# Kernel optimization log

Measured on AMD Instinct MI355X. Metric: run time of the kernel, lower is better.

Reference implementation:

```python
import jax, jax.numpy as jnp
import numpy as np

H = 64        # num_attention_heads
HK = 8        # num_key_value_heads
HD = 64       # head_dim
DM = 1024     # hidden_size
WINDOW = 128  # sliding_window


def setup_inputs() -> dict:
    key = jax.random.key(0)
    ks = jax.random.split(key, 9)
    B, S = 2, 1024
    s = 0.02
    return {
        "x": jax.random.normal(ks[0], (B, S, DM), jnp.float32),
        "Wq": jax.random.normal(ks[1], (H * HD, DM), jnp.float32) * s,
        "bq": jax.random.normal(ks[2], (H * HD,), jnp.float32) * s,
        "Wk": jax.random.normal(ks[3], (HK * HD, DM), jnp.float32) * s,
        "bk": jax.random.normal(ks[4], (HK * HD,), jnp.float32) * s,
        "Wv": jax.random.normal(ks[5], (HK * HD, DM), jnp.float32) * s,
        "bv": jax.random.normal(ks[6], (HK * HD,), jnp.float32) * s,
        "Wo": jax.random.normal(ks[7], (DM, H * HD), jnp.float32) * s,
        "bo": jax.random.normal(ks[8], (DM,), jnp.float32) * s,
        "sinks": jnp.ones((H,), jnp.float32),
    }


def reference(x, Wq, bq, Wk, bk, Wv, bv, Wo, bo, sinks):
    B, S, _ = x.shape
    G = H // HK  # GQA group size

    q = (x @ Wq.T + bq).reshape(B, S, H, HD).transpose(0, 2, 1, 3)    # [B,H,S,hd]
    k = (x @ Wk.T + bk).reshape(B, S, HK, HD).transpose(0, 2, 1, 3)   # [B,Hk,S,hd]
    v = (x @ Wv.T + bv).reshape(B, S, HK, HD).transpose(0, 2, 1, 3)
    k = jnp.repeat(k, G, axis=1)  # [B,H,S,hd]
    v = jnp.repeat(v, G, axis=1)

    scale = 1.0 / np.sqrt(HD).astype(np.float32)
    scores = jnp.einsum("bhqd,bhkd->bhqk", q, k) * scale  # [B,H,S,S]

    # causal + sliding-window mask: attend iff 0 <= q_pos - k_pos < WINDOW
    qi = jnp.arange(S)[:, None]
    kj = jnp.arange(S)[None, :]
    allowed = (qi >= kj) & (qi - kj < WINDOW)             # [S,S]
    neg = jnp.asarray(-1e30, scores.dtype)
    scores = jnp.where(allowed[None, None], scores, neg)

    # per-head learned sink logit appended as an extra softmax column
    sink = jnp.broadcast_to(sinks[None, :, None, None], (B, H, S, 1))
    logits = jnp.concatenate([scores, sink], axis=-1)      # [B,H,S,S+1]
    probs = jax.nn.softmax(logits, axis=-1)[..., :-1]      # drop sink column

    o = jnp.einsum("bhqk,bhkd->bhqd", probs, v)            # [B,H,S,hd]
    o = o.transpose(0, 2, 1, 3).reshape(B, S, H * HD)
    return o @ Wo.T + bo                                   # [B,S,DM]
```

## Files before the change

### kernel.cpp

```cpp
#include <hip/hip_runtime.h>
#include <math.h>

#define H 64
#define HK 8
#define HD 64
#define DM 1024
#define WINDOW 128
#define GQA (H / HK)
#define Bv 2
#define Sv 1024

typedef _Float16 f16;
typedef __attribute__((ext_vector_type(8))) _Float16 f16x8;
typedef __attribute__((ext_vector_type(4))) _Float16 f16x4;
typedef __attribute__((ext_vector_type(4))) float f32x4;

__device__ __forceinline__ void gload_lds16(const void* g, void* l) {
    __builtin_amdgcn_global_load_lds((const __attribute__((address_space(1))) void*)g,
                                     (__attribute__((address_space(3))) void*)l, 16, 0, 0);
}

__global__ __launch_bounds__(256, 2) void qkv_gemm(const f16* __restrict__ xh,
                                                   const f16* __restrict__ wqkv,
                                                   const float* __restrict__ bqkv,
                                                   f16* __restrict__ qh,
                                                   f16* __restrict__ khb,
                                                   f16* __restrict__ vtb) {
    __shared__ __align__(16) f16 As[128 * 64];
    __shared__ __align__(16) f16 Bs[160 * 64];

    const int t    = threadIdx.x;
    const int lane = t & 63;
    const int w    = t >> 6;
    const int lr   = lane & 15;
    const int quad = lane >> 4;
    const int srow = lane >> 3;
    const int gsw  = lane & 7;

    const int id    = blockIdx.x;
    const int s     = id >> 6;
    const int local = id & 63;
    const int bx    = (s & 3) * 8 + (local & 7);
    const int by    = (s >> 2) * 8 + (local >> 3);

    const int m0   = by * 128;
    const int n0   = bx * 160;
    const int wm   = w >> 1;
    const int wn   = w & 1;

    f32x4 acc[4][5] = {};

    for (int k0 = 0; k0 < DM; k0 += 64) {
#pragma unroll
        for (int i = 0; i < 4; ++i) {
            const int row = (w * 4 + i) * 8 + srow;
            const int g   = gsw ^ (row & 7);
            gload_lds16(xh + (size_t)(m0 + row) * DM + k0 + g * 8, As + (w * 4 + i) * 512);
        }
#pragma unroll
        for (int i = 0; i < 5; ++i) {
            const int row = (w * 5 + i) * 8 + srow;
            const int g   = gsw ^ (row & 7);
            gload_lds16(wqkv + (size_t)(n0 + row) * DM + k0 + g * 8, Bs + (w * 5 + i) * 512);
        }
        __syncthreads();
#pragma unroll
        for (int ks = 0; ks < 2; ++ks) {
            f16x8 af[4], bf[5];
#pragma unroll
            for (int tt = 0; tt < 4; ++tt) {
                const int m  = wm * 64 + tt * 16 + lr;
                const int ca = (ks * 4 + quad) ^ (m & 7);
                af[tt] = *(const f16x8*)(As + m * 64 + ca * 8);
            }
#pragma unroll
            for (int tt = 0; tt < 5; ++tt) {
                const int n  = wn * 80 + tt * 16 + lr;
                const int cb = (ks * 4 + quad) ^ (n & 7);
                bf[tt] = *(const f16x8*)(Bs + n * 64 + cb * 8);
            }
#pragma unroll
            for (int i = 0; i < 4; ++i)
#pragma unroll
                for (int j = 0; j < 5; ++j)
                    acc[i][j] = __builtin_amdgcn_mfma_f32_16x16x32_f16(af[i], bf[j], acc[i][j], 0, 0, 0);
        }
        __syncthreads();
    }

#pragma unroll
    for (int i = 0; i < 4; ++i) {
        const int grow = m0 + wm * 64 + i * 16 + quad * 4;
#pragma unroll
        for (int j = 0; j < 5; ++j) {
            const int gcb  = n0 + wn * 80 + j * 16;
            const int gcol = gcb + lr;
            const float bz = bqkv[gcol];
            if (gcb < 4096) {
#pragma unroll
                for (int r = 0; r < 4; ++r)
                    qh[(size_t)(grow + r) * 4096 + gcol] = (f16)((acc[i][j][r] + bz) * 0.125f);
            } else if (gcb < 4608) {
                const int lc = gcol - 4096;
                const size_t base = (size_t)(grow >> 10) * 524288 + (size_t)(lc >> 6) * 65536
                                  + (size_t)(grow & 1023) * 64 + (lc & 63);
#pragma unroll
                for (int r = 0; r < 4; ++r)
                    khb[base + (size_t)r * 64] = (f16)(acc[i][j][r] + bz);
            } else {
                const int lc = gcol - 4608;
                const size_t base = ((size_t)(grow >> 10) * 512 + lc) * 1024 + (grow & 1023);
                f16x4 o;
#pragma unroll
                for (int r = 0; r < 4; ++r) o[r] = (f16)(acc[i][j][r] + bz);
                *(f16x4*)(vtb + base) = o;
            }
        }
    }
}

__global__ __launch_bounds__(256, 2) void o_gemm_atomic(const f16* __restrict__ oh,
                                                        const f16* __restrict__ woh,
                                                        float* __restrict__ out) {
    __shared__ __align__(16) f16 As[128 * 64];
    __shared__ __align__(16) f16 Bs[128 * 64];

    const int t    = threadIdx.x;
    const int lane = t & 63;
    const int w    = t >> 6;
    const int lr   = lane & 15;
    const int quad = lane >> 4;
    const int srow = lane >> 3;
    const int gsw  = lane & 7;

    const int id    = blockIdx.x;
    const int kz    = id >> 7;
    const int r_    = id & 127;
    const int st    = r_ >> 6;
    const int local = r_ & 63;
    const int by    = st * 8 + (local & 7);
    const int bx    = local >> 3;

    const int m0   = by * 128;
    const int n0   = bx * 128;
    const int wm   = w >> 1;
    const int wn   = w & 1;

    const f16* A = oh  + (size_t)kz * 1024;
    const f16* W = woh + (size_t)kz * 1024;

    f32x4 acc[4][4] = {};

    for (int k0 = 0; k0 < 1024; k0 += 64) {
#pragma unroll
        for (int i = 0; i < 4; ++i) {
            const int row = (w * 4 + i) * 8 + srow;
            const int g   = gsw ^ (row & 7);
            gload_lds16(A + (size_t)(m0 + row) * 4096 + k0 + g * 8, As + (w * 4 + i) * 512);
            gload_lds16(W + (size_t)(n0 + row) * 4096 + k0 + g * 8, Bs + (w * 4 + i) * 512);
        }
        __syncthreads();
#pragma unroll
        for (int ks = 0; ks < 2; ++ks) {
            f16x8 af[4], bf[4];
#pragma unroll
            for (int tt = 0; tt < 4; ++tt) {
                const int m  = wm * 64 + tt * 16 + lr;
                const int ca = (ks * 4 + quad) ^ (m & 7);
                af[tt] = *(const f16x8*)(As + m * 64 + ca * 8);
                const int n  = wn * 64 + tt * 16 + lr;
                const int cb = (ks * 4 + quad) ^ (n & 7);
                bf[tt] = *(const f16x8*)(Bs + n * 64 + cb * 8);
            }
#pragma unroll
            for (int i = 0; i < 4; ++i)
#pragma unroll
                for (int j = 0; j < 4; ++j)
                    acc[i][j] = __builtin_amdgcn_mfma_f32_16x16x32_f16(af[i], bf[j], acc[i][j], 0, 0, 0);
        }
        __syncthreads();
    }

#pragma unroll
    for (int i = 0; i < 4; ++i) {
        const int grow = m0 + wm * 64 + i * 16 + quad * 4;
#pragma unroll
        for (int j = 0; j < 4; ++j) {
            const int gcol = n0 + wn * 64 + j * 16 + lr;
#pragma unroll
            for (int r = 0; r < 4; ++r)
                unsafeAtomicAdd(&out[(size_t)(grow + r) * 1024 + gcol], acc[i][j][r]);
        }
    }
}

#define C_X  524288
#define C_WQ 1572864
#define C_WK 1703936
#define C_WV 1835008
#define C_WO 2883584

__global__ __launch_bounds__(256) void convert_all(const float* __restrict__ x,
                                                   const float* __restrict__ Wq,
                                                   const float* __restrict__ Wk,
                                                   const float* __restrict__ Wv,
                                                   const float* __restrict__ Wo,
                                                   const float* __restrict__ bq,
                                                   const float* __restrict__ bk,
                                                   const float* __restrict__ bv,
                                                   f16* __restrict__ xh,
                                                   f16* __restrict__ wqkv,
                                                   f16* __restrict__ woh,
                                                   float* __restrict__ bqkv) {
    const int i = blockIdx.x * 256 + threadIdx.x;
    if (i < 5120) {
        float v;
        if (i < 4096)      v = bq[i];
        else if (i < 4608) v = bk[i - 4096];
        else               v = bv[i - 4608];
        bqkv[i] = v;
    }
    const float* src;
    f16* dst;
    int off;
    if (i < C_X)       { src = x;  dst = xh;              off = i; }
    else if (i < C_WQ) { src = Wq; dst = wqkv;            off = i - C_X; }
    else if (i < C_WK) { src = Wk; dst = wqkv + 4194304;  off = i - C_WQ; }
    else if (i < C_WV) { src = Wv; dst = wqkv + 4718592;  off = i - C_WK; }
    else               { src = Wo; dst = woh;             off = i - C_WV; }
    const float4 v = ((const float4*)src)[off];
    f16x4 o;
    o[0] = (f16)v.x; o[1] = (f16)v.y; o[2] = (f16)v.z; o[3] = (f16)v.w;
    *(f16x4*)(dst + (size_t)off * 4) = o;
}

#define VTS 200

__global__ __launch_bounds__(256, 2) void attn_mfma(const f16* __restrict__ qh,
                                                    const f16* __restrict__ khb,
                                                    const f16* __restrict__ vtb,
                                                    const float* __restrict__ sinks,
                                                    f16* __restrict__ oh,
                                                    const float* __restrict__ bo,
                                                    float* __restrict__ outp) {
    __shared__ __align__(16) f16 Kl[192 * 64];
    __shared__ __align__(16) f16 Vt[64 * VTS];

    const int t  = threadIdx.x;
    const int q0 = blockIdx.x * 64;
    const int hk = blockIdx.y >> 1;
    const int hh = blockIdx.y & 1;
    const int b  = blockIdx.z;
    const int c0 = q0 - WINDOW;

    {
        const int bid = (b * 16 + blockIdx.y) * 16 + blockIdx.x;
        float4* o4 = (float4*)outp;
        const float4* b4 = (const float4*)bo;
        const int base = bid * 1024 + t;
#pragma unroll
        for (int ii = 0; ii < 4; ++ii) {
            const int i = base + ii * 256;
            o4[i] = b4[i & 255];
        }
    }

    const int lane = t & 63;
    const int w    = t >> 6;
    const int lr   = lane & 15;
    const int quad = lane >> 4;
    const int srow = lane >> 3;
    const int gsw  = lane & 7;

    const f16* kg = khb + (size_t)(b * HK + hk) * Sv * HD;
    const f16* vg = vtb + (size_t)(b * HK + hk) * HD * Sv;

#pragma unroll
    for (int it = 0; it < 6; ++it) {
        const int row = (w * 6 + it) * 8 + srow;
        const int g   = gsw ^ (row & 7);
        int j = c0 + row;
        if (j < 0) j = 0;
        gload_lds16(kg + (size_t)j * HD + g * 8, Kl + (w * 6 + it) * 512);
    }
#pragma unroll
    for (int it = 0; it < 6; ++it) {
        const int i = it * 256 + t;
        const int d = i / 24, c = i % 24;
        int j0 = c0 + c * 8;
        if (j0 < 0) j0 = 0;
        const f16x8 val = *(const f16x8*)(vg + (size_t)d * Sv + j0);
        *(f16x8*)(&Vt[d * VTS + c * 8]) = val;
    }
    __syncthreads();

    const int h = hk * GQA + hh * 4 + w;

    f16x8 qf[4][2];
#pragma unroll
    for (int mt = 0; mt < 4; ++mt) {
        const f16* qrow = qh + (size_t)(b * Sv + q0 + mt * 16 + lr) * 4096 + h * 64;
#pragma unroll
        for (int ks = 0; ks < 2; ++ks)
            qf[mt][ks] = *(const f16x8*)(qrow + ks * 32 + quad * 8);
    }
    const float sk   = sinks[h];
    const int   smin = (c0 < 0) ? -c0 : 0;

    f32x4 O[4][4] = {};
    float lsum[4] = {0.f, 0.f, 0.f, 0.f};

#pragma unroll
    for (int nt = 0; nt < 12; ++nt) {
        f16x8 kf[2];
#pragma unroll
        for (int ks = 0; ks < 2; ++ks)
            kf[ks] = *(const f16x8*)(&Kl[(nt * 16 + lr) * 64 + (((ks * 4 + quad) ^ (lr & 7)) * 8)]);
        f16x4 vf[4];
#pragma unroll
        for (int dt = 0; dt < 4; ++dt)
            vf[dt] = *(const f16x4*)(&Vt[(dt * 16 + lr) * VTS + nt * 16 + quad * 4]);

#pragma unroll
        for (int mt = 0; mt < 4; ++mt) {
            if (nt < mt || nt > mt + 8) continue;
            f32x4 S = {};
#pragma unroll
            for (int ks = 0; ks < 2; ++ks)
                S = __builtin_amdgcn_mfma_f32_16x16x32_f16(kf[ks], qf[mt][ks], S, 0, 0, 0);
            f16x4 pf;
#pragma unroll
            for (int r = 0; r < 4; ++r) {
                const int sl = nt * 16 + quad * 4 + r;
                const int mq = mt * 16 + lr;
                const bool ok = (sl > mq) && (sl <= mq + WINDOW) && (sl >= smin);
                const float p = ok ? __expf(S[r]) : 0.f;
                lsum[mt] += p;
                pf[r] = (f16)p;
            }
#pragma unroll
            for (int dt = 0; dt < 4; ++dt)
                O[mt][dt] = __builtin_amdgcn_mfma_f32_16x16x16f16(vf[dt], pf, O[mt][dt], 0, 0, 0);
        }
    }

    const float esk = __expf(sk);
#pragma unroll
    for (int mt = 0; mt < 4; ++mt) {
        float l = lsum[mt];
        l += __shfl_xor(l, 16, 64);
        l += __shfl_xor(l, 32, 64);
        lsum[mt] = 1.f / (l + esk);
    }

#pragma unroll
    for (int mt = 0; mt < 4; ++mt) {
        const float inv = lsum[mt];
        f16* orow = oh + (size_t)(b * Sv + q0 + mt * 16 + lr) * 4096 + h * 64;
#pragma unroll
        for (int dt = 0; dt < 4; ++dt) {
            f16x4 ov;
#pragma unroll
            for (int r = 0; r < 4; ++r) ov[r] = (f16)(O[mt][dt][r] * inv);
            *(f16x4*)(orow + dt * 16 + quad * 4) = ov;
        }
    }
}

extern "C" void kernel_launch(void* const* d_in, const int* in_sizes, int n_in,
                              void* d_out, int out_size, void* d_ws, size_t ws_size,
                              hipStream_t stream) {
    const float* x     = (const float*)d_in[0];
    const float* Wq    = (const float*)d_in[1];
    const float* bq    = (const float*)d_in[2];
    const float* Wk    = (const float*)d_in[3];
    const float* bk    = (const float*)d_in[4];
    const float* Wv    = (const float*)d_in[5];
    const float* bv    = (const float*)d_in[6];
    const float* Wo    = (const float*)d_in[7];
    const float* bo    = (const float*)d_in[8];
    const float* sinks = (const float*)d_in[9];
    float* out = (float*)d_out;

    f16* xh   = (f16*)d_ws;
    f16* wqkv = xh + 2097152;
    f16* qh   = wqkv + 5242880;
    f16* khb  = qh + 8388608;
    f16* vtb  = khb + 1048576;
    f16* woh  = vtb + 1048576;
    f16* oh   = woh + 4194304;
    float* bqkv = (float*)(oh + 8388608);

    convert_all<<<dim3(C_WO / 256), dim3(256), 0, stream>>>(
        x, Wq, Wk, Wv, Wo, bq, bk, bv, xh, wqkv, woh, bqkv);

    qkv_gemm<<<dim3(512), dim3(256), 0, stream>>>(xh, wqkv, bqkv, qh, khb, vtb);

    attn_mfma<<<dim3(Sv / 64, HK * 2, Bv), dim3(256), 0, stream>>>(
        qh, khb, vtb, sinks, oh, bo, out);

    o_gemm_atomic<<<dim3(512), dim3(256), 0, stream>>>(oh, woh, out);
}
```

Before: 188.9 us.

## Replace split-K atomic output accumulation with partial buffers and last-block reduction

The output projection GEMM no longer accumulates its four K-slices into the output with float atomics. Each slice now writes plain stores into a workspace partial buffer and bumps a per-tile counter. The last block to finish a tile sums the four partials, adds the bias and writes the final output. Bias initialisation moves out of the attention kernel, which now only resets the counters. This trades atomic contention for extra partial-buffer traffic plus a fence and counter handshake.

```diff
diff --git a/kernel.cpp b/kernel.cpp
--- a/kernel.cpp
+++ b/kernel.cpp
@@ -119,11 +119,15 @@
     }
 }
 
-__global__ __launch_bounds__(256, 2) void o_gemm_atomic(const f16* __restrict__ oh,
-                                                        const f16* __restrict__ woh,
-                                                        float* __restrict__ out) {
+__global__ __launch_bounds__(256, 2) void o_gemm_fused(const f16* __restrict__ oh,
+                                                       const f16* __restrict__ woh,
+                                                       float* __restrict__ partials,
+                                                       int* __restrict__ ctr,
+                                                       const float* __restrict__ bo,
+                                                       float* __restrict__ out) {
     __shared__ __align__(16) f16 As[128 * 64];
     __shared__ __align__(16) f16 Bs[128 * 64];
+    __shared__ int done;
 
     const int t    = threadIdx.x;
     const int lane = t & 63;
@@ -148,6 +152,7 @@
 
     const f16* A = oh  + (size_t)kz * 1024;
     const f16* W = woh + (size_t)kz * 1024;
+    float* P = partials + (size_t)kz * 2097152;
 
     f32x4 acc[4][4] = {};
 
@@ -189,7 +194,35 @@
             const int gcol = n0 + wn * 64 + j * 16 + lr;
 #pragma unroll
             for (int r = 0; r < 4; ++r)
-                unsafeAtomicAdd(&out[(size_t)(grow + r) * 1024 + gcol], acc[i][j][r]);
+                P[(size_t)(grow + r) * 1024 + gcol] = acc[i][j][r];
+        }
+    }
+
+    const int tile = by * 8 + bx;
+    __threadfence();
+    if (t == 0) done = atomicAdd(&ctr[tile], 1);
+    __syncthreads();
+    if (done == 3) {
+        __threadfence();
+        const float4* p = (const float4*)partials;
+        const float4* b4 = (const float4*)bo;
+#pragma unroll
+        for (int ii = 0; ii < 16; ++ii) {
+            const int idx = ii * 256 + t;
+            const int rr  = idx >> 5;
+            const int cc  = idx & 31;
+            const size_t g = (size_t)(m0 + rr) * 256 + (n0 >> 2) + cc;
+            float4 a0 = p[g];
+            float4 a1 = p[g + 524288];
+            float4 a2 = p[g + 1048576];
+            float4 a3 = p[g + 1572864];
+            float4 bz = b4[(n0 >> 2) + cc];
+            float4 o;
+            o.x = a0.x + a1.x + a2.x + a3.x + bz.x;
+            o.y = a0.y + a1.y + a2.y + a3.y + bz.y;
+            o.z = a0.z + a1.z + a2.z + a3.z + bz.z;
+            o.w = a0.w + a1.w + a2.w + a3.w + bz.w;
+            ((float4*)out)[g] = o;
         }
     }
 }
@@ -241,8 +274,7 @@
                                                     const f16* __restrict__ vtb,
                                                     const float* __restrict__ sinks,
                                                     f16* __restrict__ oh,
-                                                    const float* __restrict__ bo,
-                                                    float* __restrict__ outp) {
+                                                    int* __restrict__ ctr) {
     __shared__ __align__(16) f16 Kl[192 * 64];
     __shared__ __align__(16) f16 Vt[64 * VTS];
 
@@ -253,17 +285,8 @@
     const int b  = blockIdx.z;
     const int c0 = q0 - WINDOW;
 
-    {
-        const int bid = (b * 16 + blockIdx.y) * 16 + blockIdx.x;
-        float4* o4 = (float4*)outp;
-        const float4* b4 = (const float4*)bo;
-        const int base = bid * 1024 + t;
-#pragma unroll
-        for (int ii = 0; ii < 4; ++ii) {
-            const int i = base + ii * 256;
-            o4[i] = b4[i & 255];
-        }
-    }
+    if (blockIdx.x == 0 && blockIdx.y == 0 && blockIdx.z == 0 && t < 128)
+        ctr[t] = 0;
 
     const int lane = t & 63;
     const int w    = t >> 6;
@@ -390,6 +413,8 @@
     f16* woh  = vtb + 1048576;
     f16* oh   = woh + 4194304;
     float* bqkv = (float*)(oh + 8388608);
+    int*   ctr  = (int*)(bqkv + 5120);
+    float* partials = (float*)d_ws;
 
     convert_all<<<dim3(C_WO / 256), dim3(256), 0, stream>>>(
         x, Wq, Wk, Wv, Wo, bq, bk, bv, xh, wqkv, woh, bqkv);
@@ -397,7 +422,7 @@
     qkv_gemm<<<dim3(512), dim3(256), 0, stream>>>(xh, wqkv, bqkv, qh, khb, vtb);
 
     attn_mfma<<<dim3(Sv / 64, HK * 2, Bv), dim3(256), 0, stream>>>(
-        qh, khb, vtb, sinks, oh, bo, out);
-
-    o_gemm_atomic<<<dim3(512), dim3(256), 0, stream>>>(oh, woh, out);
-}
+        qh, khb, vtb, sinks, oh, ctr);
+
+    o_gemm_fused<<<dim3(512), dim3(256), 0, stream>>>(oh, woh, partials, ctr, bo, out);
+}
```

Result: slower. 258.8 us (+37.0%).
